# Kernel tuning notes

Hardware: AMD Instinct MI355X
Metric: run time of the kernel (lower is better)

## Reference

```python
import jax, jax.numpy as jnp
import numpy as np

CE_WEIGHT = 1.0
TRIPLET_WEIGHT = 0.1
MARGIN = 0.2


def setup_inputs() -> dict:
    key = jax.random.key(0)
    k1, k2, k3 = jax.random.split(key, 3)
    B, D, V = 4096, 512, 6000
    logits = jax.random.normal(k1, (B, V), dtype=jnp.float32)
    embeddings = jax.random.normal(k2, (B, D), dtype=jnp.float32)
    labels = jax.random.randint(k3, (B,), 0, 512, dtype=jnp.int64)
    return {"logits": logits, "embeddings": embeddings, "labels": labels}


def _pairwise_dist(emb):
    # Euclidean cdist via gram matrix; safe sqrt (zero grad where d2 == 0).
    sq = jnp.sum(emb * emb, axis=-1)  # [B]
    d2 = sq[:, None] + sq[None, :] - 2.0 * (emb @ emb.T)  # [B, B]
    d2 = jnp.maximum(d2, 0.0)
    safe = jnp.where(d2 > 0.0, d2, 1.0)
    return jnp.where(d2 > 0.0, jnp.sqrt(safe), 0.0)


def _losses(logits, embeddings, labels):
    B = logits.shape[0]
    # Cross entropy (mean reduction, matching nn.CrossEntropyLoss).
    logp = jax.nn.log_softmax(logits, axis=-1)
    ce_loss = -jnp.mean(jnp.take_along_axis(logp, labels[:, None], axis=1)[:, 0])

    # Batch-hard triplet loss, fully vectorized (one masked amax/amin per row).
    dist = _pairwise_dist(embeddings)  # [B, B]
    same = labels[:, None] == labels[None, :]  # [B, B]
    eye = jnp.eye(B, dtype=bool)
    pos_mask = same & ~eye
    neg_mask = ~same
    neg_inf = jnp.float32(-np.inf)
    pos_inf = jnp.float32(np.inf)
    hardest_pos = jnp.max(jnp.where(pos_mask, dist, neg_inf), axis=1)  # [B]
    hardest_neg = jnp.min(jnp.where(neg_mask, dist, pos_inf), axis=1)  # [B]
    valid = jnp.any(pos_mask, axis=1) & jnp.any(neg_mask, axis=1)  # [B]
    per_row = jax.nn.relu(hardest_pos - hardest_neg + MARGIN)
    per_row = jnp.where(valid, per_row, 0.0)
    n_valid = jnp.sum(valid.astype(jnp.float32))
    triplet_loss = jnp.where(n_valid > 0, jnp.sum(per_row) / jnp.maximum(n_valid, 1.0), 0.0)

    total_loss = CE_WEIGHT * ce_loss + TRIPLET_WEIGHT * triplet_loss
    return total_loss, ce_loss, triplet_loss


def reference(logits, embeddings, labels):
    return _losses(logits, embeddings, labels)
```

## Files before the change

kernel.cpp:

```cpp
#include <hip/hip_runtime.h>
#include <hip/hip_bf16.h>
#include <math.h>

#define BN   4096
#define DN   512
#define VN   6000
#define NCLS 512

typedef __attribute__((ext_vector_type(8)))  short short8;
typedef __attribute__((ext_vector_type(16))) float f32x16;

__device__ __forceinline__ unsigned short f2bf(float x) {
  unsigned int u = __float_as_uint(x);
  u = (u + 0x7FFFu + ((u >> 16) & 1u)) >> 16;
  return (unsigned short)u;
}

__device__ __forceinline__ void gld_lds16(const unsigned short* g, unsigned short* l) {
  __builtin_amdgcn_global_load_lds(
      (const __attribute__((address_space(1))) void*)g,
      (__attribute__((address_space(3))) void*)l, 16, 0, 0);
}

__launch_bounds__(256)
__global__ void prep_kernel(const float* __restrict__ emb, const int* __restrict__ labels,
                            unsigned short* __restrict__ embh, float* __restrict__ sqn,
                            int* __restrict__ cnt, int* __restrict__ posb,
                            int* __restrict__ negb) {
  const int row  = blockIdx.x * 4 + (threadIdx.x >> 6);
  const int lane = threadIdx.x & 63;
  const float4* rp = (const float4*)(emb + (size_t)row * DN);
  float4 a = rp[lane];
  float4 b = rp[lane + 64];
  float ss = a.x * a.x + a.y * a.y + a.z * a.z + a.w * a.w
           + b.x * b.x + b.y * b.y + b.z * b.z + b.w * b.w;
  ushort4 ha, hb;
  ha.x = f2bf(a.x); ha.y = f2bf(a.y); ha.z = f2bf(a.z); ha.w = f2bf(a.w);
  hb.x = f2bf(b.x); hb.y = f2bf(b.y); hb.z = f2bf(b.z); hb.w = f2bf(b.w);
  ushort4* wp = (ushort4*)(embh + (size_t)row * DN);
  wp[lane] = ha;
  wp[lane + 64] = hb;
#pragma unroll
  for (int off = 1; off < 64; off <<= 1) ss += __shfl_xor(ss, off);
  if (lane == 0) {
    sqn[row] = ss;
    posb[row] = 0;
    negb[row] = 0x7F800000;
    atomicAdd(cnt + labels[row], 1);
  }
}

__device__ __forceinline__ void triplet_job(int t, unsigned short* sA, unsigned short* sB,
                                            const unsigned short* __restrict__ embh,
                                            const float* __restrict__ sqn,
                                            const int* __restrict__ labels,
                                            int* __restrict__ posb,
                                            int* __restrict__ negb, int lane) {
  const int m = lane & 31;
  const int half = lane >> 5;

  int J = (int)((sqrtf(8.f * (float)t + 1.f) - 1.f) * 0.5f);
  while ((J + 1) * (J + 2) / 2 <= t) ++J;
  while (J * (J + 1) / 2 > t) --J;
  const int I = t - J * (J + 1) / 2;
  const int i0 = I * 64, j0 = J * 64;
  const bool diag = (I == J);

  const int lrow = lane >> 3;
  const int lchk = (lane & 7) ^ lrow;
  const unsigned short* gA = embh + (size_t)(i0 + lrow) * DN + lchk * 8;
  const unsigned short* gB = embh + (size_t)(j0 + lrow) * DN + lchk * 8;

  f32x16 acc[2][2] = {};
  f32x16 accT[2][2] = {};

  for (int ks = 0; ks < 8; ++ks) {
    const int kk = ks * 64;
    asm volatile("s_waitcnt lgkmcnt(0)" ::: "memory");
#pragma unroll
    for (int s = 0; s < 8; ++s)
      gld_lds16(gA + kk + (size_t)s * 8 * DN, &sA[s * 8 * 64]);
#pragma unroll
    for (int s = 0; s < 8; ++s)
      gld_lds16(gB + kk + (size_t)s * 8 * DN, &sB[s * 8 * 64]);
    asm volatile("s_waitcnt vmcnt(0)" ::: "memory");
#pragma unroll
    for (int q = 0; q < 4; ++q) {
      const int c = q * 2 + half;
      const int sw = ((c ^ (m & 7)) * 8);
      short8 a0 = *(const short8*)&sA[m * 64 + sw];
      short8 a1 = *(const short8*)&sA[(32 + m) * 64 + sw];
      short8 b0 = *(const short8*)&sB[m * 64 + sw];
      short8 b1 = *(const short8*)&sB[(32 + m) * 64 + sw];
      acc[0][0]  = __builtin_amdgcn_mfma_f32_32x32x16_bf16(a0, b0, acc[0][0], 0, 0, 0);
      acc[0][1]  = __builtin_amdgcn_mfma_f32_32x32x16_bf16(a0, b1, acc[0][1], 0, 0, 0);
      acc[1][0]  = __builtin_amdgcn_mfma_f32_32x32x16_bf16(a1, b0, acc[1][0], 0, 0, 0);
      acc[1][1]  = __builtin_amdgcn_mfma_f32_32x32x16_bf16(a1, b1, acc[1][1], 0, 0, 0);
      accT[0][0] = __builtin_amdgcn_mfma_f32_32x32x16_bf16(b0, a0, accT[0][0], 0, 0, 0);
      accT[0][1] = __builtin_amdgcn_mfma_f32_32x32x16_bf16(b0, a1, accT[0][1], 0, 0, 0);
      accT[1][0] = __builtin_amdgcn_mfma_f32_32x32x16_bf16(b1, a0, accT[1][0], 0, 0, 0);
      accT[1][1] = __builtin_amdgcn_mfma_f32_32x32x16_bf16(b1, a1, accT[1][1], 0, 0, 0);
    }
  }

  {
    const int gj0 = j0 + m, gj1 = j0 + 32 + m;
    const int cl0 = labels[gj0], cl1 = labels[gj1];
    const float cq0 = sqn[gj0], cq1 = sqn[gj1];
    float p0 = 0.f, p1 = 0.f, n0 = INFINITY, n1 = INFINITY;
#pragma unroll
    for (int rb = 0; rb < 2; ++rb) {
#pragma unroll
      for (int r = 0; r < 16; ++r) {
        const int gi = i0 + rb * 32 + (r & 3) + 8 * (r >> 2) + 4 * half;
        const int rl = labels[gi];
        const float rq = sqn[gi];
        const float d0 = fmaf(-2.f, acc[rb][0][r], rq + cq0);
        const float d1 = fmaf(-2.f, acc[rb][1][r], rq + cq1);
        if (rl == cl0) { if (gi != gj0) p0 = fmaxf(p0, d0); } else n0 = fminf(n0, d0);
        if (rl == cl1) { if (gi != gj1) p1 = fmaxf(p1, d1); } else n1 = fminf(n1, d1);
      }
    }
    p0 = fmaxf(p0, __shfl_xor(p0, 32)); n0 = fminf(n0, __shfl_xor(n0, 32));
    p1 = fmaxf(p1, __shfl_xor(p1, 32)); n1 = fminf(n1, __shfl_xor(n1, 32));
    if (half == 0) {
      atomicMax(posb + gj0, __float_as_int(p0));
      atomicMin(negb + gj0, __float_as_int(n0));
      atomicMax(posb + gj1, __float_as_int(p1));
      atomicMin(negb + gj1, __float_as_int(n1));
    }
  }

  if (!diag) {
    const int gj0 = i0 + m, gj1 = i0 + 32 + m;
    const int cl0 = labels[gj0], cl1 = labels[gj1];
    const float cq0 = sqn[gj0], cq1 = sqn[gj1];
    float p0 = 0.f, p1 = 0.f, n0 = INFINITY, n1 = INFINITY;
#pragma unroll
    for (int rb = 0; rb < 2; ++rb) {
#pragma unroll
      for (int r = 0; r < 16; ++r) {
        const int gi = j0 + rb * 32 + (r & 3) + 8 * (r >> 2) + 4 * half;
        const int rl = labels[gi];
        const float rq = sqn[gi];
        const float d0 = fmaf(-2.f, accT[rb][0][r], rq + cq0);
        const float d1 = fmaf(-2.f, accT[rb][1][r], rq + cq1);
        if (rl == cl0) p0 = fmaxf(p0, d0); else n0 = fminf(n0, d0);
        if (rl == cl1) p1 = fmaxf(p1, d1); else n1 = fminf(n1, d1);
      }
    }
    p0 = fmaxf(p0, __shfl_xor(p0, 32)); n0 = fminf(n0, __shfl_xor(n0, 32));
    p1 = fmaxf(p1, __shfl_xor(p1, 32)); n1 = fminf(n1, __shfl_xor(n1, 32));
    if (half == 0) {
      atomicMax(posb + gj0, __float_as_int(p0));
      atomicMin(negb + gj0, __float_as_int(n0));
      atomicMax(posb + gj1, __float_as_int(p1));
      atomicMin(negb + gj1, __float_as_int(n1));
    }
  }
}

__launch_bounds__(64, 2)
__global__ void fused_kernel(const float* __restrict__ logits,
                             const int* __restrict__ labels,
                             float* __restrict__ ce_part,
                             const unsigned short* __restrict__ embh,
                             const float* __restrict__ sqn,
                             int* __restrict__ posb, int* __restrict__ negb) {
  __shared__ unsigned short smem[8192];
  const int b = blockIdx.x;
  const int lane = threadIdx.x;

  int trip_job, ce_row;
  if (b < 32) {
    trip_job = 2048 + b; ce_row = -1;
  } else {
    const int g = (b - 32) / 3, r = (b - 32) % 3;
    if (r == 0) { trip_job = g; ce_row = -1; }
    else        { trip_job = -1; ce_row = g * 2 + (r - 1); }
  }

  if (trip_job >= 0) {
    triplet_job(trip_job, smem, smem + 4096, embh, sqn, labels, posb, negb, lane);
    return;
  }

  const float* rp = logits + (size_t)ce_row * VN;
  const float xlab = rp[labels[ce_row]];
  const float4* q = (const float4*)rp;
  float4 v[24];
#pragma unroll
  for (int u = 0; u < 23; ++u) v[u] = q[lane + u * 64];
  if (lane < 28) v[23] = q[lane + 23 * 64];
  float s = 0.f;
#pragma unroll
  for (int u = 0; u < 23; ++u)
    s += __expf(v[u].x) + __expf(v[u].y) + __expf(v[u].z) + __expf(v[u].w);
  if (lane < 28)
    s += __expf(v[23].x) + __expf(v[23].y) + __expf(v[23].z) + __expf(v[23].w);
#pragma unroll
  for (int off = 1; off < 64; off <<= 1) s += __shfl_xor(s, off);
  if (lane == 0) ce_part[ce_row] = logf(s) - xlab;
}

__launch_bounds__(1024)
__global__ void finalize_kernel(const int* __restrict__ posb, const int* __restrict__ negb,
                                const int* __restrict__ labels, const int* __restrict__ cnt,
                                const float* __restrict__ ce_part, float* __restrict__ out) {
  const int tid = threadIdx.x;
  float cesum = 0.f, sum = 0.f, nv = 0.f;
#pragma unroll
  for (int u = 0; u < 4; ++u) {
    const int i = tid + u * 1024;
    cesum += ce_part[i];
    int c = cnt[labels[i]];
    float p = sqrtf(fmaxf(__int_as_float(posb[i]), 0.f));
    float n = sqrtf(fmaxf(__int_as_float(negb[i]), 0.f));
    float t = fmaxf(p - n + 0.2f, 0.f);
    if (c >= 2 && c < BN) { sum += t; nv += 1.f; }
  }
#pragma unroll
  for (int off = 1; off < 64; off <<= 1) {
    cesum += __shfl_xor(cesum, off);
    sum   += __shfl_xor(sum, off);
    nv    += __shfl_xor(nv, off);
  }
  __shared__ float s0[16], s1[16], s2[16];
  if ((tid & 63) == 0) { s0[tid >> 6] = cesum; s1[tid >> 6] = sum; s2[tid >> 6] = nv; }
  __syncthreads();
  if (tid == 0) {
    cesum = 0.f; sum = 0.f; nv = 0.f;
#pragma unroll
    for (int wv = 0; wv < 16; ++wv) { cesum += s0[wv]; sum += s1[wv]; nv += s2[wv]; }
    float trip = (nv > 0.f) ? sum / nv : 0.f;
    float ce = cesum * (1.f / BN);
    out[0] = ce + 0.1f * trip;
    out[1] = ce;
    out[2] = trip;
  }
}

extern "C" void kernel_launch(void* const* d_in, const int* in_sizes, int n_in,
                              void* d_out, int out_size, void* d_ws, size_t ws_size,
                              hipStream_t stream) {
  const float* logits = (const float*)d_in[0];
  const float* emb    = (const float*)d_in[1];
  const int*   labels = (const int*)d_in[2];
  float* out = (float*)d_out;

  char* ws = (char*)d_ws;
  unsigned short* embh = (unsigned short*)ws;
  float* sqn    = (float*)(ws + (size_t)BN * DN * 2);
  int*   posb   = (int*)((char*)sqn  + (size_t)BN * 4);
  int*   negb   = (int*)((char*)posb + (size_t)BN * 4);
  int*   cnt    = (int*)((char*)negb + (size_t)BN * 4);
  float* ce_part = (float*)((char*)cnt + (size_t)NCLS * 4);

  hipMemsetAsync(cnt, 0, (size_t)NCLS * 4, stream);
  hipLaunchKernelGGL(prep_kernel, dim3(BN / 4), dim3(256), 0, stream,
                     emb, labels, embh, sqn, cnt, posb, negb);
  hipLaunchKernelGGL(fused_kernel, dim3(32 + 2048 * 3), dim3(64), 0, stream,
                     logits, labels, ce_part, embh, sqn, posb, negb);
  hipLaunchKernelGGL(finalize_kernel, dim3(1), dim3(1024), 0, stream,
                     posb, negb, labels, cnt, ce_part, out);
}
```

Before: 181.0 us.

## Drop transposed MFMA pass; reduce row-wise via shuffles and raise occupancy

Instead of computing the transposed tile product with a second set of MFMAs to obtain per-row hardest positive/negative for off-diagonal tiles, the kernel now reduces each row of the single accumulator across the 32 lanes with xor shuffles and issues atomics per row. This halves MFMA work and accumulator registers, and launch bounds are raised to 3 blocks per CU to exploit the freed registers. In exchange it adds 32 shuffle-reduction steps of 5 shuffles each per tile plus many more atomics (one pair per row per tile), and diagonal tiles now update rows from the row-side path too, which is redundant but harmless.

Result: slower. 191.3 us (+5.7%).

```diff
diff --git a/kernel.cpp b/kernel.cpp
--- a/kernel.cpp
+++ b/kernel.cpp
@@ -64,7 +64,6 @@
   while (J * (J + 1) / 2 > t) --J;
   const int I = t - J * (J + 1) / 2;
   const int i0 = I * 64, j0 = J * 64;
-  const bool diag = (I == J);
 
   const int lrow = lane >> 3;
   const int lchk = (lane & 7) ^ lrow;
@@ -72,7 +71,6 @@
   const unsigned short* gB = embh + (size_t)(j0 + lrow) * DN + lchk * 8;
 
   f32x16 acc[2][2] = {};
-  f32x16 accT[2][2] = {};
 
   for (int ks = 0; ks < 8; ++ks) {
     const int kk = ks * 64;
@@ -92,75 +90,58 @@
       short8 a1 = *(const short8*)&sA[(32 + m) * 64 + sw];
       short8 b0 = *(const short8*)&sB[m * 64 + sw];
       short8 b1 = *(const short8*)&sB[(32 + m) * 64 + sw];
-      acc[0][0]  = __builtin_amdgcn_mfma_f32_32x32x16_bf16(a0, b0, acc[0][0], 0, 0, 0);
-      acc[0][1]  = __builtin_amdgcn_mfma_f32_32x32x16_bf16(a0, b1, acc[0][1], 0, 0, 0);
-      acc[1][0]  = __builtin_amdgcn_mfma_f32_32x32x16_bf16(a1, b0, acc[1][0], 0, 0, 0);
-      acc[1][1]  = __builtin_amdgcn_mfma_f32_32x32x16_bf16(a1, b1, acc[1][1], 0, 0, 0);
-      accT[0][0] = __builtin_amdgcn_mfma_f32_32x32x16_bf16(b0, a0, accT[0][0], 0, 0, 0);
-      accT[0][1] = __builtin_amdgcn_mfma_f32_32x32x16_bf16(b0, a1, accT[0][1], 0, 0, 0);
-      accT[1][0] = __builtin_amdgcn_mfma_f32_32x32x16_bf16(b1, a0, accT[1][0], 0, 0, 0);
-      accT[1][1] = __builtin_amdgcn_mfma_f32_32x32x16_bf16(b1, a1, accT[1][1], 0, 0, 0);
+      acc[0][0] = __builtin_amdgcn_mfma_f32_32x32x16_bf16(a0, b0, acc[0][0], 0, 0, 0);
+      acc[0][1] = __builtin_amdgcn_mfma_f32_32x32x16_bf16(a0, b1, acc[0][1], 0, 0, 0);
+      acc[1][0] = __builtin_amdgcn_mfma_f32_32x32x16_bf16(a1, b0, acc[1][0], 0, 0, 0);
+      acc[1][1] = __builtin_amdgcn_mfma_f32_32x32x16_bf16(a1, b1, acc[1][1], 0, 0, 0);
     }
   }
 
-  {
-    const int gj0 = j0 + m, gj1 = j0 + 32 + m;
-    const int cl0 = labels[gj0], cl1 = labels[gj1];
-    const float cq0 = sqn[gj0], cq1 = sqn[gj1];
-    float p0 = 0.f, p1 = 0.f, n0 = INFINITY, n1 = INFINITY;
-#pragma unroll
-    for (int rb = 0; rb < 2; ++rb) {
-#pragma unroll
-      for (int r = 0; r < 16; ++r) {
-        const int gi = i0 + rb * 32 + (r & 3) + 8 * (r >> 2) + 4 * half;
-        const int rl = labels[gi];
-        const float rq = sqn[gi];
-        const float d0 = fmaf(-2.f, acc[rb][0][r], rq + cq0);
-        const float d1 = fmaf(-2.f, acc[rb][1][r], rq + cq1);
-        if (rl == cl0) { if (gi != gj0) p0 = fmaxf(p0, d0); } else n0 = fminf(n0, d0);
-        if (rl == cl1) { if (gi != gj1) p1 = fmaxf(p1, d1); } else n1 = fminf(n1, d1);
+  const int gjc0 = j0 + m, gjc1 = j0 + 32 + m;
+  const int clab0 = labels[gjc0], clab1 = labels[gjc1];
+  const float csq0 = sqn[gjc0], csq1 = sqn[gjc1];
+  float pc0 = 0.f, pc1 = 0.f, nc0 = INFINITY, nc1 = INFINITY;
+
+#pragma unroll
+  for (int rb = 0; rb < 2; ++rb) {
+#pragma unroll
+    for (int r = 0; r < 16; ++r) {
+      const int gi = i0 + rb * 32 + (r & 3) + 8 * (r >> 2) + 4 * half;
+      const int rl = labels[gi];
+      const float rq = sqn[gi];
+      const float d0 = fmaf(-2.f, acc[rb][0][r], rq + csq0);
+      const float d1 = fmaf(-2.f, acc[rb][1][r], rq + csq1);
+      float prow = 0.f, nrow = INFINITY;
+      const bool same0 = (rl == clab0), self0 = (gi == gjc0);
+      const bool same1 = (rl == clab1), self1 = (gi == gjc1);
+      if (same0) {
+        if (!self0) { pc0 = fmaxf(pc0, d0); prow = fmaxf(prow, d0); }
+      } else { nc0 = fminf(nc0, d0); nrow = fminf(nrow, d0); }
+      if (same1) {
+        if (!self1) { pc1 = fmaxf(pc1, d1); prow = fmaxf(prow, d1); }
+      } else { nc1 = fminf(nc1, d1); nrow = fminf(nrow, d1); }
+#pragma unroll
+      for (int off = 1; off < 32; off <<= 1) {
+        prow = fmaxf(prow, __shfl_xor(prow, off));
+        nrow = fminf(nrow, __shfl_xor(nrow, off));
+      }
+      if (m == 0) {
+        atomicMax(posb + gi, __float_as_int(prow));
+        atomicMin(negb + gi, __float_as_int(nrow));
       }
     }
-    p0 = fmaxf(p0, __shfl_xor(p0, 32)); n0 = fminf(n0, __shfl_xor(n0, 32));
-    p1 = fmaxf(p1, __shfl_xor(p1, 32)); n1 = fminf(n1, __shfl_xor(n1, 32));
-    if (half == 0) {
-      atomicMax(posb + gj0, __float_as_int(p0));
-      atomicMin(negb + gj0, __float_as_int(n0));
-      atomicMax(posb + gj1, __float_as_int(p1));
-      atomicMin(negb + gj1, __float_as_int(n1));
-    }
-  }
-
-  if (!diag) {
-    const int gj0 = i0 + m, gj1 = i0 + 32 + m;
-    const int cl0 = labels[gj0], cl1 = labels[gj1];
-    const float cq0 = sqn[gj0], cq1 = sqn[gj1];
-    float p0 = 0.f, p1 = 0.f, n0 = INFINITY, n1 = INFINITY;
-#pragma unroll
-    for (int rb = 0; rb < 2; ++rb) {
-#pragma unroll
-      for (int r = 0; r < 16; ++r) {
-        const int gi = j0 + rb * 32 + (r & 3) + 8 * (r >> 2) + 4 * half;
-        const int rl = labels[gi];
-        const float rq = sqn[gi];
-        const float d0 = fmaf(-2.f, accT[rb][0][r], rq + cq0);
-        const float d1 = fmaf(-2.f, accT[rb][1][r], rq + cq1);
-        if (rl == cl0) p0 = fmaxf(p0, d0); else n0 = fminf(n0, d0);
-        if (rl == cl1) p1 = fmaxf(p1, d1); else n1 = fminf(n1, d1);
-      }
-    }
-    p0 = fmaxf(p0, __shfl_xor(p0, 32)); n0 = fminf(n0, __shfl_xor(n0, 32));
-    p1 = fmaxf(p1, __shfl_xor(p1, 32)); n1 = fminf(n1, __shfl_xor(n1, 32));
-    if (half == 0) {
-      atomicMax(posb + gj0, __float_as_int(p0));
-      atomicMin(negb + gj0, __float_as_int(n0));
-      atomicMax(posb + gj1, __float_as_int(p1));
-      atomicMin(negb + gj1, __float_as_int(n1));
-    }
-  }
-}
-
-__launch_bounds__(64, 2)
+  }
+  pc0 = fmaxf(pc0, __shfl_xor(pc0, 32)); nc0 = fminf(nc0, __shfl_xor(nc0, 32));
+  pc1 = fmaxf(pc1, __shfl_xor(pc1, 32)); nc1 = fminf(nc1, __shfl_xor(nc1, 32));
+  if (half == 0) {
+    atomicMax(posb + gjc0, __float_as_int(pc0));
+    atomicMin(negb + gjc0, __float_as_int(nc0));
+    atomicMax(posb + gjc1, __float_as_int(pc1));
+    atomicMin(negb + gjc1, __float_as_int(nc1));
+  }
+}
+
+__launch_bounds__(64, 3)
 __global__ void fused_kernel(const float* __restrict__ logits,
                              const int* __restrict__ labels,
                              float* __restrict__ ce_part,
```
